# Kernel tuning notes

Hardware: AMD Instinct MI355X
Metric: run time of the kernel (lower is better)

Reference implementation:

```python
import jax, jax.numpy as jnp
import numpy as np

B, T, HID = 4, 2048, 2048
N_HEAD, N_KV, HD = 16, 2, 128
N_REP = N_HEAD // N_KV


def setup_inputs() -> dict:
    key = jax.random.key(0)
    ks = jax.random.split(key, 7)
    s = 0.02
    return {
        "x": jax.random.normal(ks[0], (B, T, HID), jnp.float32),
        "cos": jax.random.normal(ks[1], (T, 1, HD // 2), jnp.float32),
        "sin": jax.random.normal(ks[2], (T, 1, HD // 2), jnp.float32),
        "Wq": jax.random.normal(ks[3], (N_HEAD * HD, HID), jnp.float32) * s,
        "Wk": jax.random.normal(ks[4], (N_KV * HD, HID), jnp.float32) * s,
        "Wv": jax.random.normal(ks[5], (N_KV * HD, HID), jnp.float32) * s,
        "Wo": jax.random.normal(ks[6], (HID, HID), jnp.float32) * s,
    }


def _rope(x, cos, sin):
    # x: (B, T, H, HD); cos/sin: (T, 1, HD//2) broadcast over B and H
    x_r = x[..., 0::2]
    x_i = x[..., 1::2]
    out_r = x_r * cos - x_i * sin
    out_i = x_r * sin + x_i * cos
    return jnp.stack([out_r, out_i], axis=-1).reshape(x.shape)


def _rms_norm(x):
    eps = jnp.finfo(x.dtype).eps
    var = jnp.mean(jnp.square(x), axis=-1, keepdims=True)
    return x * jax.lax.rsqrt(var + eps)


def reference(x, cos, sin, Wq, Wk, Wv, Wo):
    b, t, _ = x.shape
    q = (x @ Wq.T).reshape(b, t, N_HEAD, HD)
    k = (x @ Wk.T).reshape(b, t, N_KV, HD)
    v = (x @ Wv.T).reshape(b, t, N_KV, HD)
    q = _rms_norm(_rope(q, cos, sin))
    k = _rms_norm(_rope(k, cos, sin))
    # GQA without materializing repeated K/V: group q heads per kv head
    # q: (b, t, n_kv, n_rep, hd) -> (b, n_kv, n_rep, t, hd)
    q = q.reshape(b, t, N_KV, N_REP, HD).transpose(0, 2, 3, 1, 4)
    k = k.transpose(0, 2, 1, 3)  # (b, n_kv, t, hd)
    v = v.transpose(0, 2, 1, 3)
    scale = 1.0 / jnp.sqrt(jnp.asarray(HD, x.dtype))
    scores = jnp.einsum("bgrtd,bgsd->bgrts", q, k) * scale
    causal = jnp.tril(jnp.ones((t, t), dtype=bool))
    scores = jnp.where(causal, scores, jnp.asarray(-jnp.inf, scores.dtype))
    attn = jax.nn.softmax(scores, axis=-1)
    y = jnp.einsum("bgrts,bgsd->bgrtd", attn, v)
    # (b, n_kv, n_rep, t, hd) -> (b, t, n_head*hd)
    y = y.transpose(0, 3, 1, 2, 4).reshape(b, t, N_HEAD * HD)
    return y @ Wo.T
```

## Files before the change

### kernel.cpp

```cpp
#include <hip/hip_runtime.h>

#define B_    4
#define T_    2048
#define HID_  2048
#define NH_   16
#define NKV_  2
#define HD_   128
#define M_    (B_ * T_)
#define NQKV_ 2560

typedef __bf16 bf16x8 __attribute__((ext_vector_type(8)));
typedef float  f32x4  __attribute__((ext_vector_type(4)));

#define AS1 __attribute__((address_space(1)))
#define AS3 __attribute__((address_space(3)))

#if __has_builtin(__builtin_amdgcn_exp2f)
#define EXP2(x) __builtin_amdgcn_exp2f(x)
#else
#define EXP2(x) exp2f(x)
#endif

__device__ __forceinline__ void load_lds16(const void* g, void* l) {
  __builtin_amdgcn_global_load_lds((const AS1 unsigned int*)g,
                                   (AS3 unsigned int*)l, 16, 0, 0);
}

__device__ __forceinline__ unsigned short f2bf(float x) {
  union { float f; unsigned u; } a; a.f = x;
  unsigned r = a.u + 0x7fffu + ((a.u >> 16) & 1u);
  return (unsigned short)(r >> 16);
}
__device__ __forceinline__ float bf2f(unsigned h) {
  union { unsigned u; float f; } a; a.u = h << 16;
  return a.f;
}
__device__ __forceinline__ unsigned pk_rtz(float lo, float hi) {
  union { float f; unsigned u; } a, b; a.f = lo; b.f = hi;
  return (a.u >> 16) | (b.u & 0xffff0000u);
}

__global__ __launch_bounds__(256) void cast_bf16(const float* __restrict__ in,
                                                 unsigned short* __restrict__ out,
                                                 int n4) {
  int i = blockIdx.x * 256 + threadIdx.x;
  if (i >= n4) return;
  float4 v = ((const float4*)in)[i];
  ushort4 o;
  o.x = f2bf(v.x); o.y = f2bf(v.y); o.z = f2bf(v.z); o.w = f2bf(v.w);
  ((ushort4*)out)[i] = o;
}

__global__ __launch_bounds__(256) void cast_w(const float* __restrict__ Wq,
                                              const float* __restrict__ Wk,
                                              const float* __restrict__ Wv,
                                              unsigned short* __restrict__ out) {
  int i = blockIdx.x * 256 + threadIdx.x;
  const float* src; int j;
  if (i < 1048576)      { src = Wq; j = i; }
  else if (i < 1179648) { src = Wk; j = i - 1048576; }
  else                  { src = Wv; j = i - 1179648; }
  float4 v = ((const float4*)src)[j];
  ushort4 o;
  o.x = f2bf(v.x); o.y = f2bf(v.y); o.z = f2bf(v.z); o.w = f2bf(v.w);
  ((ushort4*)out)[i] = o;
}

template <int OUT_BF16>
__global__ __launch_bounds__(512, 1) void gemm256(const unsigned short* __restrict__ A,
                                                  const unsigned short* __restrict__ Bm,
                                                  void* __restrict__ C,
                                                  int M, int N, int K) {
  __shared__ __align__(16) unsigned short As[2][16384];
  __shared__ __align__(16) unsigned short Bs[2][16384];
  const int tid = threadIdx.x;
  const int w = tid >> 6, lane = tid & 63;
  const int wr = w >> 2, wc = w & 3;
  const int c = lane & 15, grp = lane >> 4;
  const int c7 = c & 7;
  const int m0 = blockIdx.y << 8, n0 = blockIdx.x << 8;
  const int srow = w * 8 + (lane >> 3);
  const int su = ((lane & 7) ^ ((lane >> 3) & 7)) << 3;

  f32x4 acc[8][4] = {};
  const int nkt = K >> 6;

  auto stA = [&](int h, int kt, int db) {
    const unsigned short* p = A + (size_t)(m0 + h * 128 + srow) * K + kt * 64 + su;
    load_lds16(p, &As[db][h * 8192 + (w * 8) * 64]);
    load_lds16(p + (size_t)64 * K, &As[db][h * 8192 + (64 + w * 8) * 64]);
  };
  auto stB = [&](int h, int kt, int db) {
    const unsigned short* p = Bm + (size_t)(n0 + h * 128 + srow) * K + kt * 64 + su;
    load_lds16(p, &Bs[db][h * 8192 + (w * 8) * 64]);
    load_lds16(p + (size_t)64 * K, &Bs[db][h * 8192 + (64 + w * 8) * 64]);
  };

  stA(0, 0, 0); stA(1, 0, 0); stB(0, 0, 0); stB(1, 0, 0);
  if (nkt > 1) { stB(0, 1, 1); stB(1, 1, 1); stA(0, 1, 1); }
  asm volatile("s_waitcnt vmcnt(6)" ::: "memory");
  __builtin_amdgcn_s_barrier();

  const int Abase = wr * 8192;
  const int Bbase = (wc >> 1) * 8192 + ((wc & 1) * 64) * 64;

#define RDQ(arr, mtA, mtB)                                                          \
  _Pragma("unroll")                                                                 \
  for (int ks = 0; ks < 2; ks++) {                                                  \
    arr[0][ks] = *(const bf16x8*)&Ad[((mtA) * 16 + c) * 64 + (((ks << 2) + grp) ^ c7) * 8]; \
    arr[1][ks] = *(const bf16x8*)&Ad[((mtB) * 16 + c) * 64 + (((ks << 2) + grp) ^ c7) * 8]; \
  }
#define MMQ(arr, mt0)                                                               \
  __builtin_amdgcn_s_setprio(1);                                                    \
  _Pragma("unroll")                                                                 \
  for (int ks = 0; ks < 2; ks++)                                                    \
    _Pragma("unroll")                                                               \
    for (int i = 0; i < 2; i++)                                                     \
      _Pragma("unroll")                                                             \
      for (int nt = 0; nt < 4; nt++)                                                \
        acc[(mt0) + i][nt] = __builtin_amdgcn_mfma_f32_16x16x32_bf16(               \
            arr[i][ks], b_[nt][ks], acc[(mt0) + i][nt], 0, 0, 0);                   \
  __builtin_amdgcn_s_setprio(0);

  for (int kt = 0; kt < nkt; ++kt) {
    const int db = kt & 1;
    const unsigned short* Ad = &As[db][Abase];
    const unsigned short* Bd = &Bs[db][Bbase];
    bf16x8 b_[4][2], a01[2][2], a23[2][2], a45[2][2], a67[2][2];
    RDQ(a01, 0, 1)
#pragma unroll
    for (int nt = 0; nt < 4; nt++)
#pragma unroll
      for (int ks = 0; ks < 2; ks++)
        b_[nt][ks] = *(const bf16x8*)&Bd[(nt * 16 + c) * 64 + (((ks << 2) + grp) ^ c7) * 8];
    RDQ(a23, 2, 3)
    if (kt + 1 < nkt) stA(1, kt + 1, db ^ 1);
    __builtin_amdgcn_s_barrier();
    MMQ(a01, 0)
    __builtin_amdgcn_s_barrier();
    RDQ(a45, 4, 5)
    if (kt + 2 < nkt) stB(0, kt + 2, db);
    __builtin_amdgcn_s_barrier();
    MMQ(a23, 2)
    __builtin_amdgcn_s_barrier();
    RDQ(a67, 6, 7)
    if (kt + 2 < nkt) stB(1, kt + 2, db);
    __builtin_amdgcn_s_barrier();
    MMQ(a45, 4)
    __builtin_amdgcn_s_barrier();
    if (kt + 2 < nkt) {
      stA(0, kt + 2, db);
      asm volatile("s_waitcnt vmcnt(6)" ::: "memory");
    } else {
      asm volatile("s_waitcnt vmcnt(0)" ::: "memory");
    }
    __builtin_amdgcn_s_barrier();
    MMQ(a67, 6)
    __builtin_amdgcn_s_barrier();
  }
#undef RDQ
#undef MMQ

#pragma unroll
  for (int mt = 0; mt < 8; mt++)
#pragma unroll
    for (int nt = 0; nt < 4; nt++)
#pragma unroll
      for (int r = 0; r < 4; r++) {
        int row = m0 + wr * 128 + mt * 16 + grp * 4 + r;
        int col = n0 + wc * 64 + nt * 16 + c;
        float v = acc[mt][nt][r];
        if (OUT_BF16) ((unsigned short*)C)[(size_t)row * N + col] = f2bf(v);
        else          ((float*)C)[(size_t)row * N + col] = v;
      }
}

template <int OUT_BF16>
__global__ __launch_bounds__(512, 1) void gemm256x128(const unsigned short* __restrict__ A,
                                                      const unsigned short* __restrict__ Bm,
                                                      void* __restrict__ C,
                                                      int M, int N, int K) {
  __shared__ __align__(16) unsigned short As[2][16384];
  __shared__ __align__(16) unsigned short Bs[2][8192];
  const int tid = threadIdx.x;
  const int w = tid >> 6, lane = tid & 63;
  const int wr = w >> 2, wc = w & 3;
  const int c = lane & 15, grp = lane >> 4;
  const int c7 = c & 7;
  const int m0 = blockIdx.y << 8, n0 = blockIdx.x << 7;
  const int srow = w * 8 + (lane >> 3);
  const int su = ((lane & 7) ^ ((lane >> 3) & 7)) << 3;

  f32x4 acc[8][2] = {};
  const int nkt = K >> 6;

  auto stA = [&](int h, int kt, int db) {
    const unsigned short* p = A + (size_t)(m0 + h * 128 + srow) * K + kt * 64 + su;
    load_lds16(p, &As[db][h * 8192 + (w * 8) * 64]);
    load_lds16(p + (size_t)64 * K, &As[db][h * 8192 + (64 + w * 8) * 64]);
  };
  auto stB = [&](int kt, int db) {
    const unsigned short* p = Bm + (size_t)(n0 + srow) * K + kt * 64 + su;
    load_lds16(p, &Bs[db][(w * 8) * 64]);
    load_lds16(p + (size_t)64 * K, &Bs[db][(64 + w * 8) * 64]);
  };

  stA(0, 0, 0); stA(1, 0, 0); stB(0, 0);
  if (nkt > 1) { stB(1, 1); stA(0, 1, 1); }
  asm volatile("s_waitcnt vmcnt(4)" ::: "memory");
  __builtin_amdgcn_s_barrier();

  const int Abase = wr * 8192;
  const int Bcol = wc * 32;

#define RDQ2(arr, mtA, mtB)                                                         \
  _Pragma("unroll")                                                                 \
  for (int ks = 0; ks < 2; ks++) {                                                  \
    arr[0][ks] = *(const bf16x8*)&Ad[((mtA) * 16 + c) * 64 + (((ks << 2) + grp) ^ c7) * 8]; \
    arr[1][ks] = *(const bf16x8*)&Ad[((mtB) * 16 + c) * 64 + (((ks << 2) + grp) ^ c7) * 8]; \
  }
#define MMQ2(q0, q1, mt0)                                                           \
  __builtin_amdgcn_s_setprio(1);                                                    \
  _Pragma("unroll")                                                                 \
  for (int ks = 0; ks < 2; ks++)                                                    \
    _Pragma("unroll")                                                               \
    for (int i = 0; i < 4; i++) {                                                   \
      bf16x8 av = (i < 2) ? q0[i][ks] : q1[i - 2][ks];                              \
      _Pragma("unroll")                                                             \
      for (int nt = 0; nt < 2; nt++)                                                \
        acc[(mt0) + i][nt] = __builtin_amdgcn_mfma_f32_16x16x32_bf16(               \
            av, b_[nt][ks], acc[(mt0) + i][nt], 0, 0, 0);                           \
    }                                                                               \
  __builtin_amdgcn_s_setprio(0);

  for (int kt = 0; kt < nkt; ++kt) {
    const int db = kt & 1;
    const unsigned short* Ad = &As[db][Abase];
    const unsigned short* Bd = &Bs[db][0];
    bf16x8 b_[2][2], a01[2][2], a23[2][2], a45[2][2], a67[2][2];
    RDQ2(a01, 0, 1)
#pragma unroll
    for (int nt = 0; nt < 2; nt++)
#pragma unroll
      for (int ks = 0; ks < 2; ks++)
        b_[nt][ks] = *(const bf16x8*)&Bd[(Bcol + nt * 16 + c) * 64 + (((ks << 2) + grp) ^ c7) * 8];
    RDQ2(a23, 2, 3)
    if (kt + 1 < nkt) stA(1, kt + 1, db ^ 1);
    __builtin_amdgcn_s_barrier();
    MMQ2(a01, a23, 0)
    __builtin_amdgcn_s_barrier();
    RDQ2(a45, 4, 5)
    RDQ2(a67, 6, 7)
    if (kt + 2 < nkt) {
      stB(kt + 2, db);
      stA(0, kt + 2, db);
      asm volatile("s_waitcnt vmcnt(4)" ::: "memory");
    } else {
      asm volatile("s_waitcnt vmcnt(0)" ::: "memory");
    }
    __builtin_amdgcn_s_barrier();
    MMQ2(a45, a67, 4)
    __builtin_amdgcn_s_barrier();
  }
#undef RDQ2
#undef MMQ2

#pragma unroll
  for (int mt = 0; mt < 8; mt++)
#pragma unroll
    for (int nt = 0; nt < 2; nt++)
#pragma unroll
      for (int r = 0; r < 4; r++) {
        int row = m0 + wr * 128 + mt * 16 + grp * 4 + r;
        int col = n0 + wc * 32 + nt * 16 + c;
        float v = acc[mt][nt][r];
        if (OUT_BF16) ((unsigned short*)C)[(size_t)row * N + col] = f2bf(v);
        else          ((float*)C)[(size_t)row * N + col] = v;
      }
}

__global__ __launch_bounds__(256) void rope_norm(const unsigned short* __restrict__ qkv,
                                                 const float* __restrict__ cosb,
                                                 const float* __restrict__ sinb,
                                                 unsigned short* __restrict__ qo,
                                                 unsigned short* __restrict__ ko,
                                                 unsigned short* __restrict__ vo) {
  const int m = blockIdx.x;
  const int b = m >> 11, t = m & 2047;
  const int w = threadIdx.x >> 6, lane = threadIdx.x & 63;
  const float cv = cosb[t * 64 + lane], sv = sinb[t * 64 + lane];
  const unsigned short* row = qkv + (size_t)m * NQKV_;
  const float QSCL = 0.08838834764831845f * 1.4426950408889634f;
  for (int hh = w; hh < 20; hh += 4) {
    if (hh < 18) {
      const int col0 = (hh < 16) ? hh * 128 : 2048 + (hh - 16) * 128;
      unsigned pr = *(const unsigned*)(row + col0 + 2 * lane);
      float xr = bf2f(pr & 0xffffu), xi = bf2f(pr >> 16);
      float orr = xr * cv - xi * sv;
      float oi  = xr * sv + xi * cv;
      float ss = orr * orr + oi * oi;
#pragma unroll
      for (int off = 1; off < 64; off <<= 1) ss += __shfl_xor(ss, off);
      float scl = rsqrtf(ss * (1.0f / 128.0f) + 1.1920929e-07f);
      if (hh < 16) {
        float s2 = scl * QSCL;
        unsigned out = (unsigned)f2bf(orr * s2) | ((unsigned)f2bf(oi * s2) << 16);
        *(unsigned*)(qo + (((size_t)(b * NH_ + hh)) * T_ + t) * HD_ + 2 * lane) = out;
      } else {
        unsigned out = (unsigned)f2bf(orr * scl) | ((unsigned)f2bf(oi * scl) << 16);
        *(unsigned*)(ko + (((size_t)(b * NKV_ + (hh - 16))) * T_ + t) * HD_ + 2 * lane) = out;
      }
    } else {
      const int gg = hh - 18;
      unsigned pr = *(const unsigned*)(row + 2304 + gg * 128 + 2 * lane);
      *(unsigned*)(vo + (((size_t)(b * NKV_ + gg)) * T_ + t) * HD_ + 2 * lane) = pr;
    }
  }
}

__global__ __launch_bounds__(256) void transpose_v(const unsigned short* __restrict__ v,
                                                   unsigned short* __restrict__ vt) {
  __shared__ unsigned short tile[64][65];
  const int bg = blockIdx.z;
  const int t0 = blockIdx.x << 6, h0 = blockIdx.y << 6;
  const unsigned short* src = v + (size_t)bg * T_ * HD_;
  unsigned short* dst = vt + (size_t)bg * T_ * HD_;
  const int tid = threadIdx.x;
  const int rr = tid >> 4, cc = (tid & 15) << 2;
  const int u = (cc >> 2) & 7;
  const int cp = (cc & 32) + 16 * (u & 1) + 4 * ((u >> 1) & 3);
#pragma unroll
  for (int it = 0; it < 4; it++) {
    int r = rr + it * 16;
    ushort4 d = *(const ushort4*)(src + (size_t)(t0 + r) * HD_ + h0 + cc);
    tile[r][cc + 0] = d.x; tile[r][cc + 1] = d.y;
    tile[r][cc + 2] = d.z; tile[r][cc + 3] = d.w;
  }
  __syncthreads();
#pragma unroll
  for (int it = 0; it < 4; it++) {
    int r = rr + it * 16;
    ushort4 d;
    d.x = tile[cp + 0][r]; d.y = tile[cp + 1][r];
    d.z = tile[cp + 2][r]; d.w = tile[cp + 3][r];
    *(ushort4*)(dst + (size_t)(h0 + r) * T_ + t0 + cc) = d;
  }
}

__global__ __launch_bounds__(256, 2) void flash_attn(const unsigned short* __restrict__ q,
                                                     const unsigned short* __restrict__ k,
                                                     const unsigned short* __restrict__ vt,
                                                     unsigned short* __restrict__ y) {
  __shared__ __align__(16) unsigned short Kb[2][8192];
  __shared__ __align__(16) unsigned short Vb[2][8192];
  const int tid = threadIdx.x;
  const int w = tid >> 6, lane = tid & 63;
  const int c = lane & 15, grp = lane >> 4;
  const int lr = lane >> 2;
  const int sw = (c >> 1) & 3;
  const int su = (((lane & 3) ^ ((lr >> 1) & 3)) << 3);

  const int idx = blockIdx.x;
  const int p  = idx & 7;
  const int hq = (idx >> 3) & 15;
  const int b  = idx >> 7;
  const int g  = hq >> 3;

  const unsigned short* kbase  = k  + ((size_t)(b * NKV_ + g)) * T_ * HD_;
  const unsigned short* vtbase = vt + ((size_t)(b * NKV_ + g)) * HD_ * T_;

  auto stage = [&](int s0, int bb) {
    const unsigned short* kp = kbase + (size_t)(s0 + w * 16 + lr) * HD_ + su;
#pragma unroll
    for (int dc = 0; dc < 4; dc++)
      load_lds16(kp + dc * 32, &Kb[bb][dc * 2048 + (w * 16) * 32]);
    const unsigned short* vp = vtbase + s0 + su;
#pragma unroll
    for (int ks = 0; ks < 2; ks++)
#pragma unroll
      for (int jj = 0; jj < 2; jj++)
        load_lds16(vp + (size_t)(w * 32 + jj * 16 + lr) * T_ + ks * 32,
                   &Vb[bb][ks * 4096 + (w * 32 + jj * 16) * 32]);
  };

  for (int ph = 0; ph < 2; ph++) {
    const int tile = ph ? p : (15 - p);
    const int t0 = tile << 7;
    const int t0w = t0 + w * 32;
    const unsigned short* qbase = q + (((size_t)(b * NH_ + hq)) * T_ + t0) * HD_;

    bf16x8 qf[2][4];
#pragma unroll
    for (int ti = 0; ti < 2; ti++)
#pragma unroll
      for (int ks = 0; ks < 4; ks++)
        qf[ti][ks] = *(const bf16x8*)(qbase + (size_t)(w * 32 + ti * 16 + c) * HD_ + ks * 32 + grp * 8);

    f32x4 oacc[2][8] = {};
    float mrun[2], lrun[2];
    mrun[0] = mrun[1] = -__builtin_inff();
    lrun[0] = lrun[1] = 0.f;

    const int nch = (t0 >> 6) + 2;
    stage(0, 0);
    __syncthreads();
    for (int ic = 0; ic < nch; ic++) {
      const int s0 = ic << 6, bb = ic & 1;
      if (ic + 1 < nch) stage((ic + 1) << 6, bb ^ 1);
      if (s0 <= t0w + 31) {
        const unsigned short* Kc = Kb[bb];
        const unsigned short* Vc = Vb[bb];
        f32x4 st[2][4] = {};
        __builtin_amdgcn_s_setprio(1);
#pragma unroll
        for (int s = 0; s < 4; s++)
#pragma unroll
          for (int kvt = 0; kvt < 4; kvt++) {
            bf16x8 ak = *(const bf16x8*)&Kc[s * 2048 + (kvt * 16 + c) * 32 + ((grp ^ sw) << 3)];
            st[0][kvt] = __builtin_amdgcn_mfma_f32_16x16x32_bf16(ak, qf[0][s], st[0][kvt], 0, 0, 0);
            st[1][kvt] = __builtin_amdgcn_mfma_f32_16x16x32_bf16(ak, qf[1][s], st[1][kvt], 0, 0, 0);
          }
        __builtin_amdgcn_s_setprio(0);
        if (s0 + 63 > t0w) {
#pragma unroll
          for (int ti = 0; ti < 2; ti++)
#pragma unroll
            for (int kvt = 0; kvt < 4; kvt++)
#pragma unroll
              for (int r = 0; r < 4; r++) {
                int kv = s0 + kvt * 16 + grp * 4 + r;
                int qq = t0w + ti * 16 + c;
                if (kv > qq) st[ti][kvt][r] = -__builtin_inff();
              }
        }
        unsigned pkv[2][4][2];
#pragma unroll
        for (int ti = 0; ti < 2; ti++) {
          float rm = st[ti][0][0];
#pragma unroll
          for (int kvt = 0; kvt < 4; kvt++)
#pragma unroll
            for (int r = 0; r < 4; r++) rm = fmaxf(rm, st[ti][kvt][r]);
          rm = fmaxf(rm, __shfl_xor(rm, 16));
          rm = fmaxf(rm, __shfl_xor(rm, 32));
          if (!__all(rm <= mrun[ti] + 8.f)) {
            float mnew = fmaxf(mrun[ti], rm);
            float alpha = EXP2(mrun[ti] - mnew);
            mrun[ti] = mnew;
            lrun[ti] *= alpha;
#pragma unroll
            for (int hj = 0; hj < 8; hj++)
#pragma unroll
              for (int r = 0; r < 4; r++) oacc[ti][hj][r] *= alpha;
          }
          const float m0 = mrun[ti];
          float rs = 0.f;
#pragma unroll
          for (int kvt = 0; kvt < 4; kvt++) {
            float p0 = EXP2(st[ti][kvt][0] - m0);
            float p1 = EXP2(st[ti][kvt][1] - m0);
            float p2 = EXP2(st[ti][kvt][2] - m0);
            float p3 = EXP2(st[ti][kvt][3] - m0);
            rs += (p0 + p1) + (p2 + p3);
            pkv[ti][kvt][0] = pk_rtz(p0, p1);
            pkv[ti][kvt][1] = pk_rtz(p2, p3);
          }
          rs += __shfl_xor(rs, 16);
          rs += __shfl_xor(rs, 32);
          lrun[ti] += rs;
        }
        __builtin_amdgcn_s_setprio(1);
#pragma unroll
        for (int s = 0; s < 2; s++) {
          union { int4 i; bf16x8 v; } pf0, pf1;
          pf0.i = make_int4(pkv[0][2 * s][0], pkv[0][2 * s][1], pkv[0][2 * s + 1][0], pkv[0][2 * s + 1][1]);
          pf1.i = make_int4(pkv[1][2 * s][0], pkv[1][2 * s][1], pkv[1][2 * s + 1][0], pkv[1][2 * s + 1][1]);
#pragma unroll
          for (int hj = 0; hj < 8; hj++) {
            union { int4 i; bf16x8 v; } av;
            av.i = *(const int4*)&Vc[s * 4096 + (hj * 16 + c) * 32 + ((grp ^ sw) << 3)];
            oacc[0][hj] = __builtin_amdgcn_mfma_f32_16x16x32_bf16(av.v, pf0.v, oacc[0][hj], 0, 0, 0);
            oacc[1][hj] = __builtin_amdgcn_mfma_f32_16x16x32_bf16(av.v, pf1.v, oacc[1][hj], 0, 0, 0);
          }
        }
        __builtin_amdgcn_s_setprio(0);
      }
      __syncthreads();
    }

#pragma unroll
    for (int ti = 0; ti < 2; ti++) {
      float inv = 1.f / lrun[ti];
      int trow = t0 + w * 32 + ti * 16 + c;
#pragma unroll
      for (int hj = 0; hj < 8; hj++) {
        ushort4 o;
        o.x = f2bf(oacc[ti][hj][0] * inv);
        o.y = f2bf(oacc[ti][hj][1] * inv);
        o.z = f2bf(oacc[ti][hj][2] * inv);
        o.w = f2bf(oacc[ti][hj][3] * inv);
        *(ushort4*)&y[((size_t)(b * T_ + trow)) * HID_ + hq * HD_ + hj * 16 + grp * 4] = o;
      }
    }
  }
}

extern "C" void kernel_launch(void* const* d_in, const int* in_sizes, int n_in,
                              void* d_out, int out_size, void* d_ws, size_t ws_size,
                              hipStream_t stream) {
  const float* x    = (const float*)d_in[0];
  const float* cosb = (const float*)d_in[1];
  const float* sinb = (const float*)d_in[2];
  const float* Wq   = (const float*)d_in[3];
  const float* Wk   = (const float*)d_in[4];
  const float* Wv   = (const float*)d_in[5];
  const float* Wo   = (const float*)d_in[6];
  float* out = (float*)d_out;

  char* ws = (char*)d_ws;
  size_t off = 0;
  auto take = [&](size_t elems) {
    unsigned short* p = (unsigned short*)(ws + off);
    off += ((elems * 2 + 255) & ~(size_t)255);
    return p;
  };
  unsigned short* xb   = take((size_t)M_ * HID_);
  unsigned short* wqkv = take((size_t)NQKV_ * HID_);
  unsigned short* wob  = take((size_t)HID_ * HID_);
  unsigned short* qkv  = take((size_t)M_ * NQKV_);
  unsigned short* qb   = take((size_t)B_ * NH_ * T_ * HD_);
  unsigned short* kb   = take((size_t)B_ * NKV_ * T_ * HD_);
  unsigned short* vb   = take((size_t)B_ * NKV_ * T_ * HD_);
  unsigned short* vtb  = take((size_t)B_ * NKV_ * T_ * HD_);
  unsigned short* yb   = take((size_t)M_ * HID_);
  (void)ws_size; (void)in_sizes; (void)n_in; (void)out_size;

  cast_bf16<<<16384, 256, 0, stream>>>(x, xb, 4194304);
  cast_w<<<5120, 256, 0, stream>>>(Wq, Wk, Wv, wqkv);
  cast_bf16<<<4096, 256, 0, stream>>>(Wo, wob, 1048576);

  gemm256x128<1><<<dim3(20, 32), 512, 0, stream>>>(xb, wqkv, qkv, M_, NQKV_, HID_);
  rope_norm<<<8192, 256, 0, stream>>>(qkv, cosb, sinb, qb, kb, vb);
  transpose_v<<<dim3(32, 2, 8), 256, 0, stream>>>(vb, vtb);
  flash_attn<<<dim3(512), 256, 0, stream>>>(qb, kb, vtb, yb);
  gemm256<0><<<dim3(8, 32), 512, 0, stream>>>(yb, wob, out, M_, HID_, HID_);
}
```

Before: 450.7 us.

## Widen QKV GEMM tile to 256x320 and rebalance async load schedule

Replaces the 256x128 QKV projection GEMM with a 256x320 tile, so N=2560 splits into 8 column blocks and the grid becomes 8x32 = 256 workgroups instead of 640. Each wave now computes 8x5 MFMA tiles, which raises arithmetic intensity per LDS load and reduces how often A is re-read. The global-to-LDS loads are split into 64-row pieces and spread across four phases with adjusted vmcnt waits. A wait macro with a sched_barrier is added so the compiler cannot move instructions across the waits. The larger tile costs more LDS and accumulator registers. 256 blocks may also not fill the CUs evenly.

```diff
diff --git a/kernel.cpp b/kernel.cpp
--- a/kernel.cpp
+++ b/kernel.cpp
@@ -39,6 +39,9 @@
   union { float f; unsigned u; } a, b; a.f = lo; b.f = hi;
   return (a.u >> 16) | (b.u & 0xffff0000u);
 }
+
+#define VMW_N(n) do { asm volatile("s_waitcnt vmcnt(" #n ")" ::: "memory"); \
+                      __builtin_amdgcn_sched_barrier(0); } while (0)
 
 __global__ __launch_bounds__(256) void cast_bf16(const float* __restrict__ in,
                                                  unsigned short* __restrict__ out,
@@ -98,7 +101,7 @@
 
   stA(0, 0, 0); stA(1, 0, 0); stB(0, 0, 0); stB(1, 0, 0);
   if (nkt > 1) { stB(0, 1, 1); stB(1, 1, 1); stA(0, 1, 1); }
-  asm volatile("s_waitcnt vmcnt(6)" ::: "memory");
+  VMW_N(6);
   __builtin_amdgcn_s_barrier();
 
   const int Abase = wr * 8192;
@@ -150,9 +153,9 @@
     __builtin_amdgcn_s_barrier();
     if (kt + 2 < nkt) {
       stA(0, kt + 2, db);
-      asm volatile("s_waitcnt vmcnt(6)" ::: "memory");
+      VMW_N(6);
     } else {
-      asm volatile("s_waitcnt vmcnt(0)" ::: "memory");
+      VMW_N(0);
     }
     __builtin_amdgcn_s_barrier();
     MMQ(a67, 6)
@@ -176,103 +179,110 @@
 }
 
 template <int OUT_BF16>
-__global__ __launch_bounds__(512, 1) void gemm256x128(const unsigned short* __restrict__ A,
+__global__ __launch_bounds__(512, 1) void gemm256x320(const unsigned short* __restrict__ A,
                                                       const unsigned short* __restrict__ Bm,
                                                       void* __restrict__ C,
                                                       int M, int N, int K) {
   __shared__ __align__(16) unsigned short As[2][16384];
-  __shared__ __align__(16) unsigned short Bs[2][8192];
+  __shared__ __align__(16) unsigned short Bs[2][20480];
   const int tid = threadIdx.x;
   const int w = tid >> 6, lane = tid & 63;
   const int wr = w >> 2, wc = w & 3;
   const int c = lane & 15, grp = lane >> 4;
   const int c7 = c & 7;
-  const int m0 = blockIdx.y << 8, n0 = blockIdx.x << 7;
+  const int m0 = blockIdx.y << 8, n0 = blockIdx.x * 320;
   const int srow = w * 8 + (lane >> 3);
   const int su = ((lane & 7) ^ ((lane >> 3) & 7)) << 3;
 
-  f32x4 acc[8][2] = {};
+  f32x4 acc[8][5] = {};
   const int nkt = K >> 6;
 
   auto stA = [&](int h, int kt, int db) {
-    const unsigned short* p = A + (size_t)(m0 + h * 128 + srow) * K + kt * 64 + su;
-    load_lds16(p, &As[db][h * 8192 + (w * 8) * 64]);
-    load_lds16(p + (size_t)64 * K, &As[db][h * 8192 + (64 + w * 8) * 64]);
+    load_lds16(A + (size_t)(m0 + h * 64 + srow) * K + kt * 64 + su,
+               &As[db][h * 4096 + (w * 8) * 64]);
   };
-  auto stB = [&](int kt, int db) {
-    const unsigned short* p = Bm + (size_t)(n0 + srow) * K + kt * 64 + su;
-    load_lds16(p, &Bs[db][(w * 8) * 64]);
-    load_lds16(p + (size_t)64 * K, &Bs[db][(64 + w * 8) * 64]);
+  auto stB = [&](int h, int kt, int db) {
+    load_lds16(Bm + (size_t)(n0 + h * 64 + srow) * K + kt * 64 + su,
+               &Bs[db][h * 4096 + (w * 8) * 64]);
   };
 
-  stA(0, 0, 0); stA(1, 0, 0); stB(0, 0);
-  if (nkt > 1) { stB(1, 1); stA(0, 1, 1); }
-  asm volatile("s_waitcnt vmcnt(4)" ::: "memory");
+  stA(0, 0, 0); stA(1, 0, 0); stA(2, 0, 0); stA(3, 0, 0);
+  stB(0, 0, 0); stB(1, 0, 0); stB(2, 0, 0); stB(3, 0, 0); stB(4, 0, 0);
+  if (nkt > 1) {
+    stB(0, 1, 1); stB(1, 1, 1); stB(2, 1, 1); stB(3, 1, 1); stB(4, 1, 1);
+    stA(0, 1, 1); stA(2, 1, 1);
+  }
+  VMW_N(7);
   __builtin_amdgcn_s_barrier();
 
   const int Abase = wr * 8192;
-  const int Bcol = wc * 32;
-
-#define RDQ2(arr, mtA, mtB)                                                         \
+  const int bc = wc * 80;
+
+#define RDQ3(arr, mtA, mtB)                                                         \
   _Pragma("unroll")                                                                 \
   for (int ks = 0; ks < 2; ks++) {                                                  \
     arr[0][ks] = *(const bf16x8*)&Ad[((mtA) * 16 + c) * 64 + (((ks << 2) + grp) ^ c7) * 8]; \
     arr[1][ks] = *(const bf16x8*)&Ad[((mtB) * 16 + c) * 64 + (((ks << 2) + grp) ^ c7) * 8]; \
   }
-#define MMQ2(q0, q1, mt0)                                                           \
+#define MMQ3(arr, mt0)                                                              \
   __builtin_amdgcn_s_setprio(1);                                                    \
   _Pragma("unroll")                                                                 \
   for (int ks = 0; ks < 2; ks++)                                                    \
     _Pragma("unroll")                                                               \
-    for (int i = 0; i < 4; i++) {                                                   \
-      bf16x8 av = (i < 2) ? q0[i][ks] : q1[i - 2][ks];                              \
+    for (int i = 0; i < 2; i++)                                                     \
       _Pragma("unroll")                                                             \
-      for (int nt = 0; nt < 2; nt++)                                                \
+      for (int nt = 0; nt < 5; nt++)                                                \
         acc[(mt0) + i][nt] = __builtin_amdgcn_mfma_f32_16x16x32_bf16(               \
-            av, b_[nt][ks], acc[(mt0) + i][nt], 0, 0, 0);                           \
-    }                                                                               \
+            arr[i][ks], b_[nt][ks], acc[(mt0) + i][nt], 0, 0, 0);                   \
   __builtin_amdgcn_s_setprio(0);
 
   for (int kt = 0; kt < nkt; ++kt) {
     const int db = kt & 1;
     const unsigned short* Ad = &As[db][Abase];
     const unsigned short* Bd = &Bs[db][0];
-    bf16x8 b_[2][2], a01[2][2], a23[2][2], a45[2][2], a67[2][2];
-    RDQ2(a01, 0, 1)
-#pragma unroll
-    for (int nt = 0; nt < 2; nt++)
+    bf16x8 b_[5][2], a01[2][2], a23[2][2], a45[2][2], a67[2][2];
+    RDQ3(a01, 0, 1)
+#pragma unroll
+    for (int nt = 0; nt < 5; nt++)
 #pragma unroll
       for (int ks = 0; ks < 2; ks++)
-        b_[nt][ks] = *(const bf16x8*)&Bd[(Bcol + nt * 16 + c) * 64 + (((ks << 2) + grp) ^ c7) * 8];
-    RDQ2(a23, 2, 3)
-    if (kt + 1 < nkt) stA(1, kt + 1, db ^ 1);
-    __builtin_amdgcn_s_barrier();
-    MMQ2(a01, a23, 0)
-    __builtin_amdgcn_s_barrier();
-    RDQ2(a45, 4, 5)
-    RDQ2(a67, 6, 7)
+        b_[nt][ks] = *(const bf16x8*)&Bd[(bc + nt * 16 + c) * 64 + (((ks << 2) + grp) ^ c7) * 8];
+    RDQ3(a23, 2, 3)
+    if (kt + 1 < nkt) { stA(1, kt + 1, db ^ 1); stA(3, kt + 1, db ^ 1); }
+    __builtin_amdgcn_s_barrier();
+    MMQ3(a01, 0)
+    __builtin_amdgcn_s_barrier();
+    RDQ3(a45, 4, 5)
+    if (kt + 2 < nkt) { stB(0, kt + 2, db); stB(1, kt + 2, db); }
+    __builtin_amdgcn_s_barrier();
+    MMQ3(a23, 2)
+    __builtin_amdgcn_s_barrier();
+    RDQ3(a67, 6, 7)
+    if (kt + 2 < nkt) { stB(2, kt + 2, db); stB(3, kt + 2, db); stB(4, kt + 2, db); }
+    __builtin_amdgcn_s_barrier();
+    MMQ3(a45, 4)
+    __builtin_amdgcn_s_barrier();
     if (kt + 2 < nkt) {
-      stB(kt + 2, db);
-      stA(0, kt + 2, db);
-      asm volatile("s_waitcnt vmcnt(4)" ::: "memory");
-    } else {
-      asm volatile("s_waitcnt vmcnt(0)" ::: "memory");
+      stA(0, kt + 2, db); stA(2, kt + 2, db);
+      VMW_N(7);
+    } else if (kt + 1 < nkt) {
+      VMW_N(0);
     }
     __builtin_amdgcn_s_barrier();
-    MMQ2(a45, a67, 4)
-    __builtin_amdgcn_s_barrier();
-  }
-#undef RDQ2
-#undef MMQ2
+    MMQ3(a67, 6)
+    __builtin_amdgcn_s_barrier();
+  }
+#undef RDQ3
+#undef MMQ3
 
 #pragma unroll
   for (int mt = 0; mt < 8; mt++)
 #pragma unroll
-    for (int nt = 0; nt < 2; nt++)
+    for (int nt = 0; nt < 5; nt++)
 #pragma unroll
       for (int r = 0; r < 4; r++) {
         int row = m0 + wr * 128 + mt * 16 + grp * 4 + r;
-        int col = n0 + wc * 32 + nt * 16 + c;
+        int col = n0 + wc * 80 + nt * 16 + c;
         float v = acc[mt][nt][r];
         if (OUT_BF16) ((unsigned short*)C)[(size_t)row * N + col] = f2bf(v);
         else          ((float*)C)[(size_t)row * N + col] = v;
@@ -539,7 +549,7 @@
   cast_w<<<5120, 256, 0, stream>>>(Wq, Wk, Wv, wqkv);
   cast_bf16<<<4096, 256, 0, stream>>>(Wo, wob, 1048576);
 
-  gemm256x128<1><<<dim3(20, 32), 512, 0, stream>>>(xb, wqkv, qkv, M_, NQKV_, HID_);
+  gemm256x320<1><<<dim3(8, 32), 512, 0, stream>>>(xb, wqkv, qkv, M_, NQKV_, HID_);
   rope_norm<<<8192, 256, 0, stream>>>(qkv, cosb, sinb, qb, kb, vb);
   transpose_v<<<dim3(32, 2, 8), 256, 0, stream>>>(vb, vtb);
   flash_attn<<<dim3(512), 256, 0, stream>>>(qb, kb, vtb, yb);
```

Result: slower. 481.2 us (+6.8%).
